# Performance work log

Hardware: AMD Instinct MI355X
Metric: run time of the kernel (lower is better)

The kernel has to match this reference:

```python
import jax, jax.numpy as jnp
import numpy as np


def setup_inputs() -> dict:
    key = jax.random.key(0)
    k1, k2, k3 = jax.random.split(key, 3)
    B, S, I, H, M = 8, 2048, 256, 256, 1024
    x = jax.random.normal(k1, (B, S, I), dtype=jnp.float32)
    mem = jax.random.normal(k2, (B, M, H), dtype=jnp.float32)
    # Xavier-uniform with gain=sqrt(2): bound = sqrt(2)*sqrt(6/(H+I))
    bound = np.sqrt(2.0) * np.sqrt(6.0 / (H + I))
    W = jax.random.uniform(k3, (H, I), dtype=jnp.float32, minval=-bound, maxval=bound)
    return {"x": x, "mem": mem, "W": W}


def reference(x, mem, W):
    # key[b,s,h] = relu(sum_i x[b,s,i] * W[h,i])  -- one batched GEMM for all t
    key_seq = jax.nn.relu(jnp.einsum("bsi,hi->bsh", x, W))
    # val[b,s,m] = sum_h key[b,s,h] * mem[b,m,h]
    val_seq = jnp.einsum("bsh,bmh->bsm", key_seq, mem)
    return key_seq, val_seq
```

## Files before the change

kernel.cpp:

```cpp
#include <hip/hip_runtime.h>
#include <hip/hip_bf16.h>
#include <cstdint>

typedef unsigned short u16;
typedef __bf16 bf16x8 __attribute__((ext_vector_type(8)));
typedef float f32x4 __attribute__((ext_vector_type(4)));
typedef u16 u16x8 __attribute__((ext_vector_type(8)));

#define NX 4194304L
#define NW 65536L
#define NM 2097152L
#define WS_W   (NX)
#define WS_MEM (NX + NW)
#define WS_KEY (NX + NW + NM)

__device__ __forceinline__ u16 f2bf_rne(float f) {
  union { float f; uint32_t u; } v; v.f = f;
  uint32_t r = v.u + 0x7fffu + ((v.u >> 16) & 1u);
  return (u16)(r >> 16);
}

__global__ void convert_bf16_kernel(const float* __restrict__ x,
                                    const float* __restrict__ mem,
                                    const float* __restrict__ W,
                                    u16* __restrict__ ws) {
  long e = ((long)blockIdx.x * blockDim.x + threadIdx.x) * 8;
  if (e >= NX + NW + NM) return;
  const float* src; long l;
  if (e < NX)            { src = x;   l = e; }
  else if (e < NX + NW)  { src = W;   l = e - NX; }
  else                   { src = mem; l = e - NX - NW; }
  float4 f0 = *(const float4*)(src + l);
  float4 f1 = *(const float4*)(src + l + 4);
  u16x8 o;
  o[0]=f2bf_rne(f0.x); o[1]=f2bf_rne(f0.y); o[2]=f2bf_rne(f0.z); o[3]=f2bf_rne(f0.w);
  o[4]=f2bf_rne(f1.x); o[5]=f2bf_rne(f1.y); o[6]=f2bf_rne(f1.z); o[7]=f2bf_rne(f1.w);
  *(u16x8*)(ws + e) = o;
}

#define BM 128
#define BN 128
#define BK 32

template<bool RELU, bool STORE_BF16>
__global__ __launch_bounds__(256, 2)
void gemm_nt(const u16* __restrict__ A, const u16* __restrict__ B,
             float* __restrict__ C, u16* __restrict__ Cbf,
             int M, int N, int K,
             long sA_batch, long sB_batch, long sC_batch)
{
  __shared__ __align__(16) u16 sA[BM * BK];
  __shared__ __align__(16) u16 sB[BN * BK];
  const int tid  = threadIdx.x;
  const int wave = tid >> 6;
  const int lane = tid & 63;
  const int quad = lane >> 4;
  const int r    = lane & 15;
  const int wm   = wave >> 1;
  const int wn   = wave & 1;
  const int bm   = blockIdx.y * BM;
  const int bn   = blockIdx.x * BN;
  const int batch = blockIdx.z;

  const char* Ab = (const char*)(A + (long)batch * sA_batch);
  const char* Bb = (const char*)(B + (long)batch * sB_batch);
  const long ldr = (long)K * 2;

  f32x4 acc[4][4];
  #pragma unroll
  for (int i = 0; i < 4; i++)
    #pragma unroll
    for (int j = 0; j < 4; j++)
      acc[i][j] = f32x4{0.f, 0.f, 0.f, 0.f};

  const int o0 = wave * 1024 + lane * 16;

  for (int kt = 0; kt < K; kt += BK) {
    __syncthreads();
    #pragma unroll
    for (int rr = 0; rr < 2; rr++) {
      const int o    = rr * 4096 + o0;
      const int row  = o >> 6;
      const int colb = o & 63;
      const char* ga = Ab + (long)(bm + row) * ldr + (long)kt * 2 + colb;
      const char* gb = Bb + (long)(bn + row) * ldr + (long)kt * 2 + colb;
      char* la = (char*)sA + rr * 4096 + wave * 1024;
      char* lb = (char*)sB + rr * 4096 + wave * 1024;
      __builtin_amdgcn_global_load_lds((const __attribute__((address_space(1))) void*)ga,
                                       (__attribute__((address_space(3))) void*)la, 16, 0, 0);
      __builtin_amdgcn_global_load_lds((const __attribute__((address_space(1))) void*)gb,
                                       (__attribute__((address_space(3))) void*)lb, 16, 0, 0);
    }
    __syncthreads();

    bf16x8 af[4], bf[4];
    #pragma unroll
    for (int i = 0; i < 4; i++)
      af[i] = *(const bf16x8*)(sA + (wm * 64 + i * 16 + r) * BK + quad * 8);
    #pragma unroll
    for (int j = 0; j < 4; j++)
      bf[j] = *(const bf16x8*)(sB + (wn * 64 + j * 16 + r) * BK + quad * 8);
    #pragma unroll
    for (int i = 0; i < 4; i++)
      #pragma unroll
      for (int j = 0; j < 4; j++)
        acc[i][j] = __builtin_amdgcn_mfma_f32_16x16x32_bf16(af[i], bf[j], acc[i][j], 0, 0, 0);
  }

  float* Co = C + (long)batch * sC_batch;
  u16*   Bo = STORE_BF16 ? (Cbf + (long)batch * sC_batch) : nullptr;
  #pragma unroll
  for (int i = 0; i < 4; i++) {
    #pragma unroll
    for (int j = 0; j < 4; j++) {
      #pragma unroll
      for (int reg = 0; reg < 4; reg++) {
        const int row = bm + wm * 64 + i * 16 + quad * 4 + reg;
        const int col = bn + wn * 64 + j * 16 + r;
        float v = acc[i][j][reg];
        if (RELU) v = v > 0.f ? v : 0.f;
        const long idx = (long)row * N + col;
        Co[idx] = v;
        if (STORE_BF16) Bo[idx] = f2bf_rne(v);
      }
    }
  }
}

extern "C" void kernel_launch(void* const* d_in, const int* in_sizes, int n_in,
                              void* d_out, int out_size, void* d_ws, size_t ws_size,
                              hipStream_t stream) {
  const float* x   = (const float*)d_in[0];
  const float* mem = (const float*)d_in[1];
  const float* W   = (const float*)d_in[2];
  float* out   = (float*)d_out;
  float* key_f = out;
  float* val_f = out + NX;
  u16* ws     = (u16*)d_ws;
  u16* x_bf   = ws;
  u16* W_bf   = ws + WS_W;
  u16* mem_bf = ws + WS_MEM;
  u16* key_bf = ws + WS_KEY;

  const long tot = NX + NW + NM;
  convert_bf16_kernel<<<(int)(tot / 8 / 256), 256, 0, stream>>>(x, mem, W, ws);

  dim3 g1(256 / BN, 16384 / BM, 1);
  gemm_nt<true, true><<<g1, 256, 0, stream>>>(x_bf, W_bf, key_f, key_bf,
                                              16384, 256, 256, 0, 0, 0);

  dim3 g2(1024 / BN, 2048 / BM, 8);
  gemm_nt<false, false><<<g2, 256, 0, stream>>>(key_bf, mem_bf, val_f, nullptr,
                                                2048, 1024, 256,
                                                (long)2048 * 256, (long)1024 * 256,
                                                (long)2048 * 1024);
}
```

Baseline: 127.2 us.

## Fuse fp32-to-bf16 conversion into GEMM tile loads with register prefetch

```diff
diff --git a/kernel.cpp b/kernel.cpp
--- a/kernel.cpp
+++ b/kernel.cpp
@@ -8,49 +8,29 @@
 typedef u16 u16x8 __attribute__((ext_vector_type(8)));
 
 #define NX 4194304L
-#define NW 65536L
-#define NM 2097152L
-#define WS_W   (NX)
-#define WS_MEM (NX + NW)
-#define WS_KEY (NX + NW + NM)
 
-__device__ __forceinline__ u16 f2bf_rne(float f) {
+__device__ __forceinline__ u16 f2bf(float f) {
   union { float f; uint32_t u; } v; v.f = f;
   uint32_t r = v.u + 0x7fffu + ((v.u >> 16) & 1u);
   return (u16)(r >> 16);
 }
 
-__global__ void convert_bf16_kernel(const float* __restrict__ x,
-                                    const float* __restrict__ mem,
-                                    const float* __restrict__ W,
-                                    u16* __restrict__ ws) {
-  long e = ((long)blockIdx.x * blockDim.x + threadIdx.x) * 8;
-  if (e >= NX + NW + NM) return;
-  const float* src; long l;
-  if (e < NX)            { src = x;   l = e; }
-  else if (e < NX + NW)  { src = W;   l = e - NX; }
-  else                   { src = mem; l = e - NX - NW; }
-  float4 f0 = *(const float4*)(src + l);
-  float4 f1 = *(const float4*)(src + l + 4);
+__device__ __forceinline__ u16x8 cvt8(float4 a, float4 b) {
   u16x8 o;
-  o[0]=f2bf_rne(f0.x); o[1]=f2bf_rne(f0.y); o[2]=f2bf_rne(f0.z); o[3]=f2bf_rne(f0.w);
-  o[4]=f2bf_rne(f1.x); o[5]=f2bf_rne(f1.y); o[6]=f2bf_rne(f1.z); o[7]=f2bf_rne(f1.w);
-  *(u16x8*)(ws + e) = o;
+  o[0]=f2bf(a.x); o[1]=f2bf(a.y); o[2]=f2bf(a.z); o[3]=f2bf(a.w);
+  o[4]=f2bf(b.x); o[5]=f2bf(b.y); o[6]=f2bf(b.z); o[7]=f2bf(b.w);
+  return o;
 }
 
-#define BM 128
-#define BN 128
-#define BK 32
-
-template<bool RELU, bool STORE_BF16>
+template<bool A_BF16, bool RELU, bool STORE_BF16>
 __global__ __launch_bounds__(256, 2)
-void gemm_nt(const u16* __restrict__ A, const u16* __restrict__ B,
-             float* __restrict__ C, u16* __restrict__ Cbf,
-             int M, int N, int K,
-             long sA_batch, long sB_batch, long sC_batch)
+void gemm_fused(const void* __restrict__ Ap, const float* __restrict__ Bp,
+                float* __restrict__ C, u16* __restrict__ Cbf,
+                int N, int K,
+                long sA_batch, long sB_batch, long sC_batch)
 {
-  __shared__ __align__(16) u16 sA[BM * BK];
-  __shared__ __align__(16) u16 sB[BN * BK];
+  __shared__ __align__(16) u16 sA[128 * 32];
+  __shared__ __align__(16) u16 sB[128 * 32];
   const int tid  = threadIdx.x;
   const int wave = tid >> 6;
   const int lane = tid & 63;
@@ -58,13 +38,21 @@
   const int r    = lane & 15;
   const int wm   = wave >> 1;
   const int wn   = wave & 1;
-  const int bm   = blockIdx.y * BM;
-  const int bn   = blockIdx.x * BN;
+  const int bm   = blockIdx.y * 128;
+  const int bn   = blockIdx.x * 128;
   const int batch = blockIdx.z;
 
-  const char* Ab = (const char*)(A + (long)batch * sA_batch);
-  const char* Bb = (const char*)(B + (long)batch * sB_batch);
-  const long ldr = (long)K * 2;
+  const int rowL = tid >> 1;
+  const int colL = (tid & 1) * 16;
+
+  const float* Bg = Bp + (long)batch * sB_batch + (long)(bn + rowL) * K + colL;
+  const float* Af = nullptr;
+  const u16*   Ah = nullptr;
+  if (A_BF16) Ah = (const u16*)Ap + (long)batch * sA_batch + (long)(bm + rowL) * K + colL;
+  else        Af = (const float*)Ap + (long)batch * sA_batch + (long)(bm + rowL) * K + colL;
+
+  u16* dA = sA + rowL * 32 + colL;
+  u16* dB = sB + rowL * 32 + colL;
 
   f32x4 acc[4][4];
   #pragma unroll
@@ -73,33 +61,60 @@
     for (int j = 0; j < 4; j++)
       acc[i][j] = f32x4{0.f, 0.f, 0.f, 0.f};
 
-  const int o0 = wave * 1024 + lane * 16;
+  float4 ra[4], rb[4];
+  uint4  ha[2];
 
-  for (int kt = 0; kt < K; kt += BK) {
+  if (A_BF16) {
+    ha[0] = *(const uint4*)(Ah);
+    ha[1] = *(const uint4*)(Ah + 8);
+  } else {
+    ra[0] = *(const float4*)(Af);
+    ra[1] = *(const float4*)(Af + 4);
+    ra[2] = *(const float4*)(Af + 8);
+    ra[3] = *(const float4*)(Af + 12);
+  }
+  rb[0] = *(const float4*)(Bg);
+  rb[1] = *(const float4*)(Bg + 4);
+  rb[2] = *(const float4*)(Bg + 8);
+  rb[3] = *(const float4*)(Bg + 12);
+
+  for (int kt = 0; kt < K; kt += 32) {
     __syncthreads();
-    #pragma unroll
-    for (int rr = 0; rr < 2; rr++) {
-      const int o    = rr * 4096 + o0;
-      const int row  = o >> 6;
-      const int colb = o & 63;
-      const char* ga = Ab + (long)(bm + row) * ldr + (long)kt * 2 + colb;
-      const char* gb = Bb + (long)(bn + row) * ldr + (long)kt * 2 + colb;
-      char* la = (char*)sA + rr * 4096 + wave * 1024;
-      char* lb = (char*)sB + rr * 4096 + wave * 1024;
-      __builtin_amdgcn_global_load_lds((const __attribute__((address_space(1))) void*)ga,
-                                       (__attribute__((address_space(3))) void*)la, 16, 0, 0);
-      __builtin_amdgcn_global_load_lds((const __attribute__((address_space(1))) void*)gb,
-                                       (__attribute__((address_space(3))) void*)lb, 16, 0, 0);
+    if (A_BF16) {
+      *(uint4*)dA       = ha[0];
+      *(uint4*)(dA + 8) = ha[1];
+    } else {
+      *(u16x8*)dA       = cvt8(ra[0], ra[1]);
+      *(u16x8*)(dA + 8) = cvt8(ra[2], ra[3]);
     }
+    *(u16x8*)dB       = cvt8(rb[0], rb[1]);
+    *(u16x8*)(dB + 8) = cvt8(rb[2], rb[3]);
     __syncthreads();
+
+    const int kn = kt + 32;
+    if (kn < K) {
+      if (A_BF16) {
+        ha[0] = *(const uint4*)(Ah + kn);
+        ha[1] = *(const uint4*)(Ah + kn + 8);
+      } else {
+        ra[0] = *(const float4*)(Af + kn);
+        ra[1] = *(const float4*)(Af + kn + 4);
+        ra[2] = *(const float4*)(Af + kn + 8);
+        ra[3] = *(const float4*)(Af + kn + 12);
+      }
+      rb[0] = *(const float4*)(Bg + kn);
+      rb[1] = *(const float4*)(Bg + kn + 4);
+      rb[2] = *(const float4*)(Bg + kn + 8);
+      rb[3] = *(const float4*)(Bg + kn + 12);
+    }
 
     bf16x8 af[4], bf[4];
     #pragma unroll
     for (int i = 0; i < 4; i++)
-      af[i] = *(const bf16x8*)(sA + (wm * 64 + i * 16 + r) * BK + quad * 8);
+      af[i] = *(const bf16x8*)(sA + (wm * 64 + i * 16 + r) * 32 + quad * 8);
     #pragma unroll
     for (int j = 0; j < 4; j++)
-      bf[j] = *(const bf16x8*)(sB + (wn * 64 + j * 16 + r) * BK + quad * 8);
+      bf[j] = *(const bf16x8*)(sB + (wn * 64 + j * 16 + r) * 32 + quad * 8);
     #pragma unroll
     for (int i = 0; i < 4; i++)
       #pragma unroll
@@ -121,7 +136,7 @@
         if (RELU) v = v > 0.f ? v : 0.f;
         const long idx = (long)row * N + col;
         Co[idx] = v;
-        if (STORE_BF16) Bo[idx] = f2bf_rne(v);
+        if (STORE_BF16) Bo[idx] = f2bf(v);
       }
     }
   }
@@ -136,22 +151,14 @@
   float* out   = (float*)d_out;
   float* key_f = out;
   float* val_f = out + NX;
-  u16* ws     = (u16*)d_ws;
-  u16* x_bf   = ws;
-  u16* W_bf   = ws + WS_W;
-  u16* mem_bf = ws + WS_MEM;
-  u16* key_bf = ws + WS_KEY;
+  u16* key_bf  = (u16*)d_ws;
 
-  const long tot = NX + NW + NM;
-  convert_bf16_kernel<<<(int)(tot / 8 / 256), 256, 0, stream>>>(x, mem, W, ws);
+  dim3 g1(2, 128, 1);
+  gemm_fused<false, true, true><<<g1, 256, 0, stream>>>(
+      (const void*)x, W, key_f, key_bf, 256, 256, 0, 0, 0);
 
-  dim3 g1(256 / BN, 16384 / BM, 1);
-  gemm_nt<true, true><<<g1, 256, 0, stream>>>(x_bf, W_bf, key_f, key_bf,
-                                              16384, 256, 256, 0, 0, 0);
-
-  dim3 g2(1024 / BN, 2048 / BM, 8);
-  gemm_nt<false, false><<<g2, 256, 0, stream>>>(key_bf, mem_bf, val_f, nullptr,
-                                                2048, 1024, 256,
-                                                (long)2048 * 256, (long)1024 * 256,
-                                                (long)2048 * 1024);
+  dim3 g2(8, 16, 8);
+  gemm_fused<true, false, false><<<g2, 256, 0, stream>>>(
+      (const void*)key_bf, mem, val_f, nullptr, 1024, 256,
+      (long)2048 * 256, (long)1024 * 256, (long)2048 * 1024);
 }
```

After: 149.6 us. +17.6%, slower.
